# Performance work log

Measured on AMD Instinct MI355X. Metric: run time of the kernel, lower is better.

## Reference

```python
import jax, jax.numpy as jnp
import numpy as np

TEMPERATURE = 0.5
B, D = 4096, 256


def setup_inputs() -> dict:
    key = jax.random.key(0)
    k1, k2 = jax.random.split(key)
    z_i = jax.random.normal(k1, (B, D), dtype=jnp.float32)
    z_j = jax.random.normal(k2, (B, D), dtype=jnp.float32)
    return {"z_i": z_i, "z_j": z_j}


def reference(z_i, z_j):
    batch = z_i.shape[0]
    n = 2 * batch
    z = jnp.concatenate([z_i, z_j], axis=0)                      # [2B, D]
    z = z / jnp.linalg.norm(z, axis=1, keepdims=True)            # L2-normalize rows
    # cosine_similarity of unit vectors == dot product -> single GEMM
    sim = jnp.einsum('id,jd->ij', z, z) / TEMPERATURE            # [2B, 2B]
    mask = jnp.eye(n, dtype=bool)
    sim = jnp.where(mask, -jnp.inf, sim)                         # mask self-similarity
    positives = jnp.concatenate(
        [jnp.diagonal(sim, offset=batch), jnp.diagonal(sim, offset=-batch)], axis=0
    )                                                            # [2B]
    loss = -positives + jax.nn.logsumexp(sim, axis=1)            # [2B]
    return loss.mean()
```

## Files before the change

kernel.cpp:

```cpp
#include <hip/hip_runtime.h>
#include <hip/hip_bf16.h>
#include <stdint.h>
#include <stddef.h>


#define B_ROWS 4096
#define D_DIM  256
#define N_ROWS 8192
#define BM 128
#define BN 64

typedef __bf16 bf16;
typedef bf16  bf16x8  __attribute__((ext_vector_type(8)));
typedef bf16  bf16x4  __attribute__((ext_vector_type(4)));
typedef float floatx4 __attribute__((ext_vector_type(4)));

__global__ __launch_bounds__(256) void normalize_kernel(
    const float* __restrict__ z_i, const float* __restrict__ z_j,
    bf16* __restrict__ zn, float* __restrict__ sumexp) {
  const int wave = threadIdx.x >> 6;
  const int lane = threadIdx.x & 63;
  const int row  = blockIdx.x * 4 + wave;
  const float* src = (row < B_ROWS) ? (z_i + (size_t)row * D_DIM)
                                    : (z_j + (size_t)(row - B_ROWS) * D_DIM);
  float4 v = ((const float4*)src)[lane];
  float ss = v.x * v.x + v.y * v.y + v.z * v.z + v.w * v.w;
  #pragma unroll
  for (int m = 1; m < 64; m <<= 1) ss += __shfl_xor(ss, m);
  const float rn = rsqrtf(ss);
  bf16x4 o;
  o[0] = (bf16)(v.x * rn);
  o[1] = (bf16)(v.y * rn);
  o[2] = (bf16)(v.z * rn);
  o[3] = (bf16)(v.w * rn);
  ((bf16x4*)(zn + (size_t)row * D_DIM))[lane] = o;
  if (lane == 0) sumexp[row] = 0.f;
}

__global__ __launch_bounds__(256, 2) void simexp_kernel(
    const bf16* __restrict__ zn, float* __restrict__ sumexp,
    float* __restrict__ pos) {
  __shared__ __align__(16) bf16 Bs[2][BN * D_DIM];

  const int tid   = threadIdx.x;
  const int wave  = tid >> 6;
  const int lane  = tid & 63;
  const int lcol  = lane & 15;
  const int lquad = lane >> 4;
  const int wr = (wave >> 1) * 64;
  const int wc = (wave & 1) * 32;
  const int ri = blockIdx.x >> 3;
  const int cj = blockIdx.x & 7;
  const int row_base = ri * BM;
  const int jt0 = cj * 16;

  auto stageB = [&](int buf, int jt) {
    const bf16* src = zn + (size_t)jt * BN * D_DIM;
    #pragma unroll
    for (int it = 0; it < 8; ++it) {
      const int s   = it * 256 + tid;
      const int n   = s >> 5;
      const int kcs = s & 31;
      const int kc  = (kcs & 24) | ((kcs & 7) ^ (n & 7));
      __builtin_amdgcn_global_load_lds(
          (const __attribute__((address_space(1))) unsigned int*)
              (src + (size_t)n * D_DIM + kc * 8),
          (__attribute__((address_space(3))) unsigned int*)&Bs[buf][s * 8],
          16, 0, 0);
    }
  };

  stageB(0, jt0);

  floatx4 af[4][8];
  #pragma unroll
  for (int ti = 0; ti < 4; ++ti) {
    const bf16* arow =
        zn + (size_t)(row_base + wr + ti * 16 + lcol) * D_DIM + lquad * 8;
    #pragma unroll
    for (int kq = 0; kq < 8; ++kq)
      af[ti][kq] = *(const floatx4*)(arow + kq * 32);
  }

  float rowsum[4][4];
  #pragma unroll
  for (int ti = 0; ti < 4; ++ti)
    #pragma unroll
    for (int r = 0; r < 4; ++r) rowsum[ti][r] = 0.f;

  #pragma unroll 1
  for (int t = 0; t < 16; ++t) {
    const int jt = jt0 + t;
    __syncthreads();
    if (t < 15) stageB((t + 1) & 1, jt + 1);

    floatx4 acc[4][2];
    #pragma unroll
    for (int ti = 0; ti < 4; ++ti)
      #pragma unroll
      for (int tj = 0; tj < 2; ++tj) acc[ti][tj] = floatx4{0.f, 0.f, 0.f, 0.f};

    const bf16* bbase = &Bs[t & 1][0];
    #pragma unroll
    for (int kq = 0; kq < 8; ++kq) {
      const int kc  = kq * 4 + lquad;
      const int kcs = (kc & 24) | ((kc & 7) ^ (lcol & 7));
      bf16x8 bfr[2];
      #pragma unroll
      for (int tj = 0; tj < 2; ++tj) {
        const int n = wc + tj * 16 + lcol;
        bfr[tj] = *(const bf16x8*)(bbase + n * D_DIM + kcs * 8);
      }
      #pragma unroll
      for (int ti = 0; ti < 4; ++ti)
        #pragma unroll
        for (int tj = 0; tj < 2; ++tj)
          acc[ti][tj] = __builtin_amdgcn_mfma_f32_16x16x32_bf16(
              __builtin_bit_cast(bf16x8, af[ti][kq]), bfr[tj], acc[ti][tj],
              0, 0, 0);
    }

    const int jth = jt >> 1;
    const bool special = (jth == ri) || (jth == ri + 32) || (jth + 32 == ri);
    const int col_base = jt * BN;
    #pragma unroll
    for (int ti = 0; ti < 4; ++ti) {
      #pragma unroll
      for (int tj = 0; tj < 2; ++tj) {
        #pragma unroll
        for (int r = 0; r < 4; ++r) {
          const float v = acc[ti][tj][r];
          float e = __builtin_amdgcn_exp2f(v * 2.8853900817779268f);
          if (special) {
            const int rg = row_base + wr + ti * 16 + lquad * 4 + r;
            const int cg = col_base + wc + tj * 16 + lcol;
            if (cg == rg) e = 0.f;
            else if (cg == rg + B_ROWS || cg + B_ROWS == rg)
              pos[rg] = 2.0f * v;
          }
          rowsum[ti][r] += e;
        }
      }
    }
  }

  #pragma unroll
  for (int ti = 0; ti < 4; ++ti) {
    #pragma unroll
    for (int r = 0; r < 4; ++r) {
      float s = rowsum[ti][r];
      s += __shfl_xor(s, 1);
      s += __shfl_xor(s, 2);
      s += __shfl_xor(s, 4);
      s += __shfl_xor(s, 8);
      if (lcol == 0) {
        const int grow = row_base + wr + ti * 16 + lquad * 4 + r;
        atomicAdd(&sumexp[grow], s);
      }
    }
  }
}

__global__ __launch_bounds__(1024) void reduce_kernel(
    const float* __restrict__ sumexp, const float* __restrict__ pos,
    float* __restrict__ out) {
  __shared__ float ws[16];
  const int tid = threadIdx.x;
  float s = 0.f;
  const float ln2 = 0.6931471805599453f;
  for (int k = tid; k < N_ROWS; k += 1024)
    s += __builtin_amdgcn_logf(sumexp[k]) * ln2 - pos[k];
  #pragma unroll
  for (int m = 1; m < 64; m <<= 1) s += __shfl_xor(s, m);
  const int wave = tid >> 6, lane = tid & 63;
  if (lane == 0) ws[wave] = s;
  __syncthreads();
  if (wave == 0) {
    float t = (lane < 16) ? ws[lane] : 0.f;
    #pragma unroll
    for (int m = 1; m < 16; m <<= 1) t += __shfl_xor(t, m);
    if (lane == 0) out[0] = t * (1.0f / N_ROWS);
  }
}

extern "C" void kernel_launch(void* const* d_in, const int* in_sizes, int n_in,
                              void* d_out, int out_size, void* d_ws,
                              size_t ws_size, hipStream_t stream) {
  const float* z_i = (const float*)d_in[0];
  const float* z_j = (const float*)d_in[1];
  float* out = (float*)d_out;

  bf16* zn = (bf16*)d_ws;
  float* sumexp = (float*)((char*)d_ws + (size_t)N_ROWS * D_DIM * sizeof(bf16));
  float* pos = sumexp + N_ROWS;

  normalize_kernel<<<N_ROWS / 4, 256, 0, stream>>>(z_i, z_j, zn, sumexp);
  simexp_kernel<<<(N_ROWS / BM) * 8, 256, 0, stream>>>(zn, sumexp, pos);
  reduce_kernel<<<1, 1024, 0, stream>>>(sumexp, pos, out);
}
```

Before: 104.4 us.

## Exploit similarity matrix symmetry to compute only upper half of tiles

Each row block now visits only a cyclic half of the column tiles (plus a tie-breaking extra for the middle diagonal), and each computed tile contributes exp sums both to its rows and, through column reductions and atomics, to its columns. This roughly halves the MFMA and exp work of the GEMM-plus-exp kernel. In exchange it adds per-tile column shuffles and extra global atomics, and the grid stays at 512 blocks with uneven iteration counts (8 or 10) across blocks.

New measurement: 100.3 us. -3.9%, faster.

```diff
diff --git a/kernel.cpp b/kernel.cpp
--- a/kernel.cpp
+++ b/kernel.cpp
@@ -52,7 +52,11 @@
   const int ri = blockIdx.x >> 3;
   const int cj = blockIdx.x & 7;
   const int row_base = ri * BM;
-  const int jt0 = cj * 16;
+  const int niter = (cj == 7 && ri < 32) ? 10 : 8;
+
+  auto jt64 = [&](int it) {
+    return 2 * ((ri + 4 * cj + (it >> 1)) & 63) + (it & 1);
+  };
 
   auto stageB = [&](int buf, int jt) {
     const bf16* src = zn + (size_t)jt * BN * D_DIM;
@@ -70,7 +74,7 @@
     }
   };
 
-  stageB(0, jt0);
+  stageB(0, jt64(0));
 
   floatx4 af[4][8];
   #pragma unroll
@@ -89,10 +93,9 @@
     for (int r = 0; r < 4; ++r) rowsum[ti][r] = 0.f;
 
   #pragma unroll 1
-  for (int t = 0; t < 16; ++t) {
-    const int jt = jt0 + t;
+  for (int t = 0; t < niter; ++t) {
     __syncthreads();
-    if (t < 15) stageB((t + 1) & 1, jt + 1);
+    if (t + 1 < niter) stageB((t + 1) & 1, jt64(t + 1));
 
     floatx4 acc[4][2];
     #pragma unroll
@@ -120,9 +123,12 @@
               0, 0, 0);
     }
 
-    const int jth = jt >> 1;
-    const bool special = (jth == ri) || (jth == ri + 32) || (jth + 32 == ri);
+    const int s    = 4 * cj + (t >> 1);
+    const bool diag = (s == 0);
+    const bool posT = (s == 32);
+    const int jt = jt64(t);
     const int col_base = jt * BN;
+    float colsum[2] = {0.f, 0.f};
     #pragma unroll
     for (int ti = 0; ti < 4; ++ti) {
       #pragma unroll
@@ -131,31 +137,45 @@
         for (int r = 0; r < 4; ++r) {
           const float v = acc[ti][tj][r];
           float e = __builtin_amdgcn_exp2f(v * 2.8853900817779268f);
-          if (special) {
+          if (diag || posT) {
             const int rg = row_base + wr + ti * 16 + lquad * 4 + r;
             const int cg = col_base + wc + tj * 16 + lcol;
-            if (cg == rg) e = 0.f;
-            else if (cg == rg + B_ROWS || cg + B_ROWS == rg)
+            if (diag && cg == rg) e = 0.f;
+            if (posT && cg == rg + B_ROWS) {
               pos[rg] = 2.0f * v;
+              pos[cg] = 2.0f * v;
+            }
           }
           rowsum[ti][r] += e;
+          colsum[tj]    += e;
         }
       }
     }
+
+    if (!diag) {
+      #pragma unroll
+      for (int tj = 0; tj < 2; ++tj) {
+        float cs = colsum[tj];
+        cs += __shfl_xor(cs, 16);
+        cs += __shfl_xor(cs, 32);
+        if (lquad == 0)
+          atomicAdd(&sumexp[col_base + wc + tj * 16 + lcol], cs);
+      }
+    }
   }
 
   #pragma unroll
   for (int ti = 0; ti < 4; ++ti) {
     #pragma unroll
     for (int r = 0; r < 4; ++r) {
-      float s = rowsum[ti][r];
-      s += __shfl_xor(s, 1);
-      s += __shfl_xor(s, 2);
-      s += __shfl_xor(s, 4);
-      s += __shfl_xor(s, 8);
+      float s2 = rowsum[ti][r];
+      s2 += __shfl_xor(s2, 1);
+      s2 += __shfl_xor(s2, 2);
+      s2 += __shfl_xor(s2, 4);
+      s2 += __shfl_xor(s2, 8);
       if (lcol == 0) {
         const int grow = row_base + wr + ti * 16 + lquad * 4 + r;
-        atomicAdd(&sumexp[grow], s);
+        atomicAdd(&sumexp[grow], s2);
       }
     }
   }
@@ -195,6 +215,6 @@
   float* pos = sumexp + N_ROWS;
 
   normalize_kernel<<<N_ROWS / 4, 256, 0, stream>>>(z_i, z_j, zn, sumexp);
-  simexp_kernel<<<(N_ROWS / BM) * 8, 256, 0, stream>>>(zn, sumexp, pos);
+  simexp_kernel<<<512, 256, 0, stream>>>(zn, sumexp, pos);
   reduce_kernel<<<1, 1024, 0, stream>>>(sumexp, pos, out);
 }
```
